# Optimization experiments

Measured on AMD Instinct MI355X. Metric: run time of the kernel, lower is better.

The kernel has to match this reference:

```python
import jax, jax.numpy as jnp
import numpy as np

NG, NT, E = 2500, 20000, 640000
SRC_DIM, DST_DIM, HID, OUT, NCLS = 128, 500, 128, 128, 16


def setup_inputs() -> dict:
    key = jax.random.key(0)
    ks = jax.random.split(key, 11)
    d = {
        "gene_feats": jax.random.normal(ks[0], (NG, SRC_DIM), jnp.float32),
        "train_feats": jax.random.normal(ks[1], (NT, DST_DIM), jnp.float32),
        "edge_src": jax.random.randint(ks[2], (E,), 0, NG),
        "edge_dst": jax.random.randint(ks[3], (E,), 0, NT),
        # conv1: SAGEConv((src_dim, dst_dim) -> hidden)
        "W1_neigh": jax.random.normal(ks[4], (SRC_DIM, HID), jnp.float32) / np.sqrt(SRC_DIM),
        "W1_self": jax.random.normal(ks[5], (DST_DIM, HID), jnp.float32) / np.sqrt(DST_DIM),
        "b1": jnp.zeros((HID,), jnp.float32),
        # conv2: SAGEConv(hidden -> out); src input is the raw gene features
        "W2_neigh": jax.random.normal(ks[6], (HID, OUT), jnp.float32) / np.sqrt(HID),
        "W2_self": jax.random.normal(ks[7], (HID, OUT), jnp.float32) / np.sqrt(HID),
        "b2": jnp.zeros((OUT,), jnp.float32),
        # classifier MLP
        "Wc1": jax.random.normal(ks[8], (OUT, OUT), jnp.float32) / np.sqrt(OUT),
        "bc1": jnp.zeros((OUT,), jnp.float32),
        "Wc2": jax.random.normal(ks[9], (OUT, NCLS), jnp.float32) / np.sqrt(OUT),
        "bc2": jnp.zeros((NCLS,), jnp.float32),
    }
    return d


def _segment_mean(msgs, dst, num_segments):
    # mean over in-edges; isolated dst nodes get 0 (DGL convention)
    sums = jax.ops.segment_sum(msgs, dst, num_segments=num_segments)
    cnt = jax.ops.segment_sum(jnp.ones((msgs.shape[0],), msgs.dtype), dst,
                              num_segments=num_segments)
    return sums / jnp.maximum(cnt, 1.0)[:, None]


def reference(gene_feats, train_feats, edge_src, edge_dst,
              W1_neigh, W1_self, b1, W2_neigh, W2_self, b2,
              Wc1, bc1, Wc2, bc2):
    # mean-aggregate gene (src) features onto train (dst) nodes
    agg = _segment_mean(gene_feats[edge_src], edge_dst, NT)  # [NT, SRC_DIM]
    # conv1: fc_self(h_dst) + fc_neigh(mean_neigh) + bias, then ReLU
    h1 = jax.nn.relu(train_feats @ W1_self + agg @ W1_neigh + b1)  # [NT, HID]
    # conv2 reuses raw gene features as src -> same mean aggregation
    h2 = jax.nn.relu(h1 @ W2_self + agg @ W2_neigh + b2)  # [NT, OUT]
    # classifier: Linear -> ReLU -> Linear
    return jax.nn.relu(h2 @ Wc1 + bc1) @ Wc2 + bc2  # [NT, NCLS]
```

## Files before the change

### kernel.cpp

```cpp
#include <hip/hip_runtime.h>


#define NG 2500
#define NT 20000
#define NE 640000
#define NCLS 16
#define CAP 96

typedef unsigned short u16;
typedef unsigned int u32;

typedef float f32x4 __attribute__((ext_vector_type(4)));
typedef __bf16 bf16x8 __attribute__((ext_vector_type(8)));

__device__ __forceinline__ float b2f(u16 u) { return __uint_as_float(((u32)u) << 16); }
__device__ __forceinline__ float blo(u32 p) { return __uint_as_float(p << 16); }
__device__ __forceinline__ float bhi(u32 p) { return __uint_as_float(p & 0xffff0000u); }
__device__ __forceinline__ u16 f2b(float f) {
    u32 u = __float_as_uint(f);
    return (u16)((u + 0x7fffu + ((u >> 16) & 1u)) >> 16);
}

#define B1N 81920
#define B2N 32768
#define B3N 16384
#define B4N 2048
#define NEB 625
#define GNB 625
#define PKB 520

__global__ __launch_bounds__(256) void k_prep(
    const int* __restrict__ esrc, const int* __restrict__ edst,
    int* __restrict__ cnt, u16* __restrict__ csr,
    const float* __restrict__ gene, u32* __restrict__ GH32,
    const float* __restrict__ W1n, const float* __restrict__ W1s,
    const float* __restrict__ W2n, const float* __restrict__ W2s,
    const float* __restrict__ Wc1, const float* __restrict__ Wc2,
    u16* __restrict__ B1h, u16* __restrict__ B1l,
    u16* __restrict__ B2h, u16* __restrict__ B2l,
    u16* __restrict__ B3h, u16* __restrict__ B3l,
    u16* __restrict__ B4h, u16* __restrict__ B4l) {
    int blk = blockIdx.x, t = threadIdx.x;
    if (blk < NEB) {
        int e0 = (blk * 256 + t) * 4;
        const int4 s4 = *(const int4*)(esrc + e0);
        const int4 d4 = *(const int4*)(edst + e0);
        int ss[4] = {s4.x, s4.y, s4.z, s4.w};
        int dd[4] = {d4.x, d4.y, d4.z, d4.w};
#pragma unroll
        for (int i = 0; i < 4; ++i) {
            unsigned d = (unsigned)dd[i];
            if (d < NT) {
                int slot = atomicAdd(&cnt[d], 1);
                if (slot < CAP) csr[(size_t)d * CAP + slot] = (u16)ss[i];
            }
        }
        return;
    }
    if (blk < NEB + GNB) {
        int idx = (blk - NEB) * 256 + t;
        float2 v = ((const float2*)gene)[idx];
        GH32[idx] = (u32)f2b(v.x) | ((u32)f2b(v.y) << 16);
        return;
    }
    int idx = (blk - NEB - GNB) * 256 + t;
    float v = 0.f;
    u16 *ph = 0, *pl = 0;
    int off = 0;
    if (idx < B1N) {
        int j = idx & 7, l = (idx >> 3) & 63, rest = idx >> 9;
        int g = rest & 7, kk = rest >> 3;
        int k = kk * 32 + ((l >> 4) << 3) + j, n = (g << 4) + (l & 15);
        if (k < 500) v = W1s[k * 128 + n];
        else if (k >= 512) v = W1n[(k - 512) * 128 + n];
        ph = B1h; pl = B1l; off = idx;
    } else if (idx < B1N + B2N) {
        int e = idx - B1N;
        int j = e & 7, l = (e >> 3) & 63, rest = e >> 9;
        int g = rest & 7, kk = rest >> 3;
        int k = kk * 32 + ((l >> 4) << 3) + j, n = (g << 4) + (l & 15);
        v = (k < 128) ? W2s[k * 128 + n] : W2n[(k - 128) * 128 + n];
        ph = B2h; pl = B2l; off = e;
    } else if (idx < B1N + B2N + B3N) {
        int e = idx - (B1N + B2N);
        int j = e & 7, l = (e >> 3) & 63, rest = e >> 9;
        int g = rest & 7, kk = rest >> 3;
        int k = kk * 32 + ((l >> 4) << 3) + j, n = (g << 4) + (l & 15);
        v = Wc1[k * 128 + n];
        ph = B3h; pl = B3l; off = e;
    } else if (idx < B1N + B2N + B3N + B4N) {
        int e = idx - (B1N + B2N + B3N);
        int j = e & 7, l = (e >> 3) & 63, kk = e >> 9;
        int k = kk * 32 + ((l >> 4) << 3) + j, n = l & 15;
        v = Wc2[k * 16 + n];
        ph = B4h; pl = B4l; off = e;
    }
    if (ph) {
        u16 hi = f2b(v);
        u16 lo = f2b(v - b2f(hi));
        ph[off] = hi;
        pl[off] = lo;
    }
}

__global__ __launch_bounds__(512, 3) void k_mega(
    const int* __restrict__ cnt, const u16* __restrict__ csr,
    const u16* __restrict__ GH, const float* __restrict__ train,
    const u16* __restrict__ B1h, const u16* __restrict__ B1l,
    const u16* __restrict__ B2h, const u16* __restrict__ B2l,
    const u16* __restrict__ B3h, const u16* __restrict__ B3l,
    const u16* __restrict__ B4h, const u16* __restrict__ B4l,
    const float* __restrict__ b1, const float* __restrict__ b2,
    const float* __restrict__ bc1, const float* __restrict__ bc2,
    float* __restrict__ out) {
    __shared__ __align__(16) u16 SMEM[26112];
    u16* SAGh = SMEM;
    u16* SAGl = SMEM + 4352;
    u16* S1h = SMEM + 8704;
    u16* S1l = SMEM + 13056;
    u16* S2h = SMEM + 17408;
    u16* S2l = SMEM + 21760;
    u16* TS = SMEM + 8704;

    int t = threadIdx.x;
    int row0 = blockIdx.x * 32;

    float4 st[8];
    {
        const float4* tb = (const float4*)(train + (size_t)row0 * 500);
#pragma unroll
        for (int i = 0; i < 7; ++i) st[i] = tb[t + i * 512];
        if (t < 416) st[7] = tb[t + 3584];
    }

    int gr = t >> 4, cg = t & 15;
    int d = row0 + gr;
    int ctrue = cnt[d];
    int c = ctrue > CAP ? CAP : ctrue;
    const u16* crow = csr + (size_t)d * CAP;
    int nfull = c >> 3;
    uint4 i40 = *(const uint4*)(crow);
    uint4 i41 = *(const uint4*)(crow + 8);
    uint4 i42 = *(const uint4*)(crow + 16);
    uint4 i43 = *(const uint4*)(crow + 24);
    float a[8];
#pragma unroll
    for (int p = 0; p < 8; ++p) a[p] = 0.f;

    {
        u32* T32 = (u32*)TS;
#pragma unroll
        for (int i = 0; i < 8; ++i) {
            int idx = t + i * 512;
            if (i == 7 && t >= 416) break;
            int r = idx / 125, c4 = idx - r * 125;
            int base = r * 260 + c4 * 2;
            T32[base] = (u32)f2b(st[i].x) | ((u32)f2b(st[i].y) << 16);
            T32[base + 1] = (u32)f2b(st[i].z) | ((u32)f2b(st[i].w) << 16);
        }
        if (t < 192) {
            int r = t / 6, c4 = t - r * 6;
            T32[r * 260 + 250 + c4] = 0;
        }
    }
    __syncthreads();

    int lane = t & 63, g = t >> 6;
    int m = lane & 15, q = lane >> 4, n16 = lane & 15;

    int hr0 = m * 136 + q * 8;
    int hr1 = (16 + m) * 136 + q * 8;
    int cr0 = q * 4, cr1 = 16 + q * 4;
    const f32x4 z4 = {0.f, 0.f, 0.f, 0.f};
    f32x4 acc0 = z4, acc1 = z4;
    const u16* tA0 = TS + m * 520 + q * 8;
    const u16* tA1 = TS + (16 + m) * 520 + q * 8;

#define ACC(p)                                      \
    do {                                            \
        a[0] += blo((p).x); a[1] += bhi((p).x);     \
        a[2] += blo((p).y); a[3] += bhi((p).y);     \
        a[4] += blo((p).z); a[5] += bhi((p).z);     \
        a[6] += blo((p).w); a[7] += bhi((p).w);     \
    } while (0)

    auto GHLoad = [&](int s) -> uint4 {
        return *(const uint4*)(GH + (size_t)s * 128 + cg * 8);
    };
    uint4 P0, P1, P2, P3, P4, P5, P6, P7;
    auto issue8 = [&](uint4 iq) {
        P0 = GHLoad((int)(iq.x & 0xffffu)); P1 = GHLoad((int)(iq.x >> 16));
        P2 = GHLoad((int)(iq.y & 0xffffu)); P3 = GHLoad((int)(iq.y >> 16));
        P4 = GHLoad((int)(iq.z & 0xffffu)); P5 = GHLoad((int)(iq.z >> 16));
        P6 = GHLoad((int)(iq.w & 0xffffu)); P7 = GHLoad((int)(iq.w >> 16));
    };
    auto acc8 = [&]() {
        ACC(P0); ACC(P1); ACC(P2); ACC(P3);
        ACC(P4); ACC(P5); ACC(P6); ACC(P7);
    };
    auto kk4 = [&](int base) {
#pragma unroll
        for (int kk = base; kk < base + 4; ++kk) {
            bf16x8 a0 = *(const bf16x8*)(tA0 + kk * 32);
            bf16x8 a1 = *(const bf16x8*)(tA1 + kk * 32);
            size_t bo = ((size_t)(kk * 8 + g) * 64 + lane) * 8;
            bf16x8 bh = *(const bf16x8*)(B1h + bo);
            bf16x8 bl = *(const bf16x8*)(B1l + bo);
            acc0 = __builtin_amdgcn_mfma_f32_16x16x32_bf16(a0, bh, acc0, 0, 0, 0);
            acc0 = __builtin_amdgcn_mfma_f32_16x16x32_bf16(a0, bl, acc0, 0, 0, 0);
            acc1 = __builtin_amdgcn_mfma_f32_16x16x32_bf16(a1, bh, acc1, 0, 0, 0);
            acc1 = __builtin_amdgcn_mfma_f32_16x16x32_bf16(a1, bl, acc1, 0, 0, 0);
        }
    };

    if (nfull > 0) issue8(i40);
    kk4(0);
    if (nfull > 0) acc8();
    if (nfull > 1) issue8(i41);
    kk4(4);
    if (nfull > 1) acc8();
    if (nfull > 2) issue8(i42);
    kk4(8);
    if (nfull > 2) acc8();
    if (nfull > 3) issue8(i43);
    kk4(12);
    if (nfull > 3) acc8();
    for (int b = 4; b < nfull; ++b) {
        uint4 i4 = *(const uint4*)(crow + b * 8);
        issue8(i4);
        acc8();
    }
    {
        int j = nfull * 8;
        if (j < c) {
            uint4 i4 = *(const uint4*)(crow + j);
            u32 w[4] = {i4.x, i4.y, i4.z, i4.w};
#pragma unroll
            for (int k = 0; k < 8; ++k) {
                int s = (int)((w[k >> 1] >> ((k & 1) * 16)) & 0xffffu);
                bool live = (j + k) < c;
                s = live ? s : 0;
                uint4 p = GHLoad(s);
                if (live) ACC(p);
            }
        }
    }
#undef ACC

    {
        float inv = (ctrue > 0) ? 1.f / (float)ctrue : 0.f;
        int base = (gr * 136 + cg * 8) >> 1;
        u32* SH = (u32*)SAGh;
        u32* SL = (u32*)SAGl;
#pragma unroll
        for (int p = 0; p < 4; ++p) {
            float x = a[2 * p] * inv, y = a[2 * p + 1] * inv;
            u16 hx = f2b(x), hy = f2b(y);
            SH[base + p] = (u32)hx | ((u32)hy << 16);
            SL[base + p] = (u32)f2b(x - b2f(hx)) | ((u32)f2b(y - b2f(hy)) << 16);
        }
    }
    __syncthreads();

#pragma unroll
    for (int kk = 16; kk < 20; ++kk) {
        int o = (kk - 16) * 32;
        bf16x8 ah0 = *(const bf16x8*)(SAGh + hr0 + o);
        bf16x8 al0 = *(const bf16x8*)(SAGl + hr0 + o);
        bf16x8 ah1 = *(const bf16x8*)(SAGh + hr1 + o);
        bf16x8 al1 = *(const bf16x8*)(SAGl + hr1 + o);
        size_t bo = ((size_t)(kk * 8 + g) * 64 + lane) * 8;
        bf16x8 bh = *(const bf16x8*)(B1h + bo);
        bf16x8 bl = *(const bf16x8*)(B1l + bo);
        acc0 = __builtin_amdgcn_mfma_f32_16x16x32_bf16(ah0, bh, acc0, 0, 0, 0);
        acc0 = __builtin_amdgcn_mfma_f32_16x16x32_bf16(ah0, bl, acc0, 0, 0, 0);
        acc0 = __builtin_amdgcn_mfma_f32_16x16x32_bf16(al0, bh, acc0, 0, 0, 0);
        acc1 = __builtin_amdgcn_mfma_f32_16x16x32_bf16(ah1, bh, acc1, 0, 0, 0);
        acc1 = __builtin_amdgcn_mfma_f32_16x16x32_bf16(ah1, bl, acc1, 0, 0, 0);
        acc1 = __builtin_amdgcn_mfma_f32_16x16x32_bf16(al1, bh, acc1, 0, 0, 0);
    }
    {
        int n = g * 16 + n16;
        float bias = b1[n];
#pragma unroll
        for (int rg = 0; rg < 4; ++rg) {
            float v0 = acc0[rg] + bias; v0 = v0 > 0.f ? v0 : 0.f;
            float v1 = acc1[rg] + bias; v1 = v1 > 0.f ? v1 : 0.f;
            u16 h0 = f2b(v0), h1v = f2b(v1);
            S1h[(cr0 + rg) * 136 + n] = h0; S1l[(cr0 + rg) * 136 + n] = f2b(v0 - b2f(h0));
            S1h[(cr1 + rg) * 136 + n] = h1v; S1l[(cr1 + rg) * 136 + n] = f2b(v1 - b2f(h1v));
        }
    }
    __syncthreads();

    acc0 = z4; acc1 = z4;
#pragma unroll
    for (int kk = 0; kk < 8; ++kk) {
        const u16* Ph = (kk < 4) ? S1h : SAGh;
        const u16* Pl = (kk < 4) ? S1l : SAGl;
        int o = (kk & 3) * 32;
        bf16x8 ah0 = *(const bf16x8*)(Ph + hr0 + o);
        bf16x8 al0 = *(const bf16x8*)(Pl + hr0 + o);
        bf16x8 ah1 = *(const bf16x8*)(Ph + hr1 + o);
        bf16x8 al1 = *(const bf16x8*)(Pl + hr1 + o);
        size_t bo = ((size_t)(kk * 8 + g) * 64 + lane) * 8;
        bf16x8 bh = *(const bf16x8*)(B2h + bo);
        bf16x8 bl = *(const bf16x8*)(B2l + bo);
        acc0 = __builtin_amdgcn_mfma_f32_16x16x32_bf16(ah0, bh, acc0, 0, 0, 0);
        acc0 = __builtin_amdgcn_mfma_f32_16x16x32_bf16(ah0, bl, acc0, 0, 0, 0);
        acc0 = __builtin_amdgcn_mfma_f32_16x16x32_bf16(al0, bh, acc0, 0, 0, 0);
        acc1 = __builtin_amdgcn_mfma_f32_16x16x32_bf16(ah1, bh, acc1, 0, 0, 0);
        acc1 = __builtin_amdgcn_mfma_f32_16x16x32_bf16(ah1, bl, acc1, 0, 0, 0);
        acc1 = __builtin_amdgcn_mfma_f32_16x16x32_bf16(al1, bh, acc1, 0, 0, 0);
    }
    {
        int n = g * 16 + n16;
        float bias = b2[n];
#pragma unroll
        for (int rg = 0; rg < 4; ++rg) {
            float v0 = acc0[rg] + bias; v0 = v0 > 0.f ? v0 : 0.f;
            float v1 = acc1[rg] + bias; v1 = v1 > 0.f ? v1 : 0.f;
            u16 h0 = f2b(v0), h1v = f2b(v1);
            S2h[(cr0 + rg) * 136 + n] = h0; S2l[(cr0 + rg) * 136 + n] = f2b(v0 - b2f(h0));
            S2h[(cr1 + rg) * 136 + n] = h1v; S2l[(cr1 + rg) * 136 + n] = f2b(v1 - b2f(h1v));
        }
    }
    __syncthreads();

    acc0 = z4; acc1 = z4;
#pragma unroll
    for (int kk = 0; kk < 4; ++kk) {
        int o = kk * 32;
        bf16x8 ah0 = *(const bf16x8*)(S2h + hr0 + o);
        bf16x8 al0 = *(const bf16x8*)(S2l + hr0 + o);
        bf16x8 ah1 = *(const bf16x8*)(S2h + hr1 + o);
        bf16x8 al1 = *(const bf16x8*)(S2l + hr1 + o);
        size_t bo = ((size_t)(kk * 8 + g) * 64 + lane) * 8;
        bf16x8 bh = *(const bf16x8*)(B3h + bo);
        bf16x8 bl = *(const bf16x8*)(B3l + bo);
        acc0 = __builtin_amdgcn_mfma_f32_16x16x32_bf16(ah0, bh, acc0, 0, 0, 0);
        acc0 = __builtin_amdgcn_mfma_f32_16x16x32_bf16(ah0, bl, acc0, 0, 0, 0);
        acc0 = __builtin_amdgcn_mfma_f32_16x16x32_bf16(al0, bh, acc0, 0, 0, 0);
        acc1 = __builtin_amdgcn_mfma_f32_16x16x32_bf16(ah1, bh, acc1, 0, 0, 0);
        acc1 = __builtin_amdgcn_mfma_f32_16x16x32_bf16(ah1, bl, acc1, 0, 0, 0);
        acc1 = __builtin_amdgcn_mfma_f32_16x16x32_bf16(al1, bh, acc1, 0, 0, 0);
    }
    {
        int n = g * 16 + n16;
        float bias = bc1[n];
#pragma unroll
        for (int rg = 0; rg < 4; ++rg) {
            float v0 = acc0[rg] + bias; v0 = v0 > 0.f ? v0 : 0.f;
            float v1 = acc1[rg] + bias; v1 = v1 > 0.f ? v1 : 0.f;
            u16 h0 = f2b(v0), h1v = f2b(v1);
            S1h[(cr0 + rg) * 136 + n] = h0; S1l[(cr0 + rg) * 136 + n] = f2b(v0 - b2f(h0));
            S1h[(cr1 + rg) * 136 + n] = h1v; S1l[(cr1 + rg) * 136 + n] = f2b(v1 - b2f(h1v));
        }
    }
    __syncthreads();

    if (g < 2) {
        int hr = (g == 0) ? hr0 : hr1;
        int cr = (g == 0) ? cr0 : cr1;
        f32x4 a4 = z4;
#pragma unroll
        for (int kk = 0; kk < 4; ++kk) {
            bf16x8 ah = *(const bf16x8*)(S1h + hr + kk * 32);
            bf16x8 al = *(const bf16x8*)(S1l + hr + kk * 32);
            size_t bo = ((size_t)kk * 64 + lane) * 8;
            bf16x8 bh = *(const bf16x8*)(B4h + bo);
            bf16x8 bl = *(const bf16x8*)(B4l + bo);
            a4 = __builtin_amdgcn_mfma_f32_16x16x32_bf16(ah, bh, a4, 0, 0, 0);
            a4 = __builtin_amdgcn_mfma_f32_16x16x32_bf16(ah, bl, a4, 0, 0, 0);
            a4 = __builtin_amdgcn_mfma_f32_16x16x32_bf16(al, bh, a4, 0, 0, 0);
        }
        float bias = bc2[n16];
#pragma unroll
        for (int rg = 0; rg < 4; ++rg)
            out[(size_t)(row0 + cr + rg) * NCLS + n16] = a4[rg] + bias;
    }
}

extern "C" void kernel_launch(void* const* d_in, const int* in_sizes, int n_in,
                              void* d_out, int out_size, void* d_ws, size_t ws_size,
                              hipStream_t stream) {
    const float* gene = (const float*)d_in[0];
    const float* train = (const float*)d_in[1];
    const int* esrc = (const int*)d_in[2];
    const int* edst = (const int*)d_in[3];

    char* ws = (char*)d_ws;
    int* cnt = (int*)(ws + 0);
    u16* csr = (u16*)(ws + 80000);
    u16* GH = (u16*)(ws + 3920000);
    u16* B1h = (u16*)(ws + 4560000);
    u16* B1l = (u16*)(ws + 4723840);
    u16* B2h = (u16*)(ws + 4887680);
    u16* B2l = (u16*)(ws + 4953216);
    u16* B3h = (u16*)(ws + 5018752);
    u16* B3l = (u16*)(ws + 5051520);
    u16* B4h = (u16*)(ws + 5084288);
    u16* B4l = (u16*)(ws + 5088384);

    hipMemsetAsync(cnt, 0, NT * sizeof(int), stream);
    k_prep<<<NEB + GNB + PKB, 256, 0, stream>>>(
        esrc, edst, cnt, csr, gene, (u32*)GH,
        (const float*)d_in[4], (const float*)d_in[5], (const float*)d_in[7],
        (const float*)d_in[8], (const float*)d_in[10], (const float*)d_in[12],
        B1h, B1l, B2h, B2l, B3h, B3l, B4h, B4l);
    k_mega<<<NT / 32, 512, 0, stream>>>(
        cnt, csr, GH, train, B1h, B1l, B2h, B2l, B3h, B3l, B4h, B4l,
        (const float*)d_in[6], (const float*)d_in[9], (const float*)d_in[11],
        (const float*)d_in[13], (float*)d_out);
}
```

Baseline: 172.5 us.

## Bucket edges per 32-row block and build per-row lists in shared memory

Result: slower. 313.0 us (+81.5%).

```diff
diff --git a/kernel.cpp b/kernel.cpp
--- a/kernel.cpp
+++ b/kernel.cpp
@@ -6,6 +6,7 @@
 #define NE 640000
 #define NCLS 16
 #define CAP 96
+#define BCAP 1536
 
 typedef unsigned short u16;
 typedef unsigned int u32;
@@ -31,7 +32,7 @@
 
 __global__ __launch_bounds__(256) void k_prep(
     const int* __restrict__ esrc, const int* __restrict__ edst,
-    int* __restrict__ cnt, u16* __restrict__ csr,
+    int* __restrict__ bcnt, u32* __restrict__ bkt,
     const float* __restrict__ gene, u32* __restrict__ GH32,
     const float* __restrict__ W1n, const float* __restrict__ W1s,
     const float* __restrict__ W2n, const float* __restrict__ W2s,
@@ -51,8 +52,10 @@
         for (int i = 0; i < 4; ++i) {
             unsigned d = (unsigned)dd[i];
             if (d < NT) {
-                int slot = atomicAdd(&cnt[d], 1);
-                if (slot < CAP) csr[(size_t)d * CAP + slot] = (u16)ss[i];
+                int b = (int)(d >> 5);
+                int pos = atomicAdd(&bcnt[b], 1);
+                if (pos < BCAP)
+                    bkt[(size_t)b * BCAP + pos] = ((d & 31u) << 16) | (u32)ss[i];
             }
         }
         return;
@@ -104,7 +107,7 @@
 }
 
 __global__ __launch_bounds__(512, 3) void k_mega(
-    const int* __restrict__ cnt, const u16* __restrict__ csr,
+    const int* __restrict__ bcnt, const u32* __restrict__ bkt,
     const u16* __restrict__ GH, const float* __restrict__ train,
     const u16* __restrict__ B1h, const u16* __restrict__ B1l,
     const u16* __restrict__ B2h, const u16* __restrict__ B2l,
@@ -114,6 +117,8 @@
     const float* __restrict__ bc1, const float* __restrict__ bc2,
     float* __restrict__ out) {
     __shared__ __align__(16) u16 SMEM[26112];
+    __shared__ __align__(16) u16 SRT[32 * CAP];
+    __shared__ int POS[32];
     u16* SAGh = SMEM;
     u16* SAGl = SMEM + 4352;
     u16* S1h = SMEM + 8704;
@@ -133,19 +138,17 @@
         if (t < 416) st[7] = tb[t + 3584];
     }
 
-    int gr = t >> 4, cg = t & 15;
-    int d = row0 + gr;
-    int ctrue = cnt[d];
-    int c = ctrue > CAP ? CAP : ctrue;
-    const u16* crow = csr + (size_t)d * CAP;
-    int nfull = c >> 3;
-    uint4 i40 = *(const uint4*)(crow);
-    uint4 i41 = *(const uint4*)(crow + 8);
-    uint4 i42 = *(const uint4*)(crow + 16);
-    uint4 i43 = *(const uint4*)(crow + 24);
-    float a[8];
-#pragma unroll
-    for (int p = 0; p < 8; ++p) a[p] = 0.f;
+    if (t < 32) POS[t] = 0;
+    int bc = bcnt[blockIdx.x];
+    if (bc > BCAP) bc = BCAP;
+    __syncthreads();
+
+    for (int i = t; i < bc; i += 512) {
+        u32 e = bkt[(size_t)blockIdx.x * BCAP + i];
+        int r = (int)(e >> 16);
+        int p = atomicAdd(&POS[r], 1);
+        if (p < CAP) SRT[r * CAP + p] = (u16)(e & 0xffffu);
+    }
 
     {
         u32* T32 = (u32*)TS;
@@ -167,6 +170,19 @@
 
     int lane = t & 63, g = t >> 6;
     int m = lane & 15, q = lane >> 4, n16 = lane & 15;
+    int gr = t >> 4, cg = t & 15;
+
+    int ctrue = POS[gr];
+    int c = ctrue > CAP ? CAP : ctrue;
+    const u16* crow = SRT + gr * CAP;
+    int nfull = c >> 3;
+    uint4 i40 = *(const uint4*)(crow);
+    uint4 i41 = *(const uint4*)(crow + 8);
+    uint4 i42 = *(const uint4*)(crow + 16);
+    uint4 i43 = *(const uint4*)(crow + 24);
+    float a[8];
+#pragma unroll
+    for (int p = 0; p < 8; ++p) a[p] = 0.f;
 
     int hr0 = m * 136 + q * 8;
     int hr1 = (16 + m) * 136 + q * 8;
@@ -390,26 +406,26 @@
     const int* edst = (const int*)d_in[3];
 
     char* ws = (char*)d_ws;
-    int* cnt = (int*)(ws + 0);
-    u16* csr = (u16*)(ws + 80000);
-    u16* GH = (u16*)(ws + 3920000);
-    u16* B1h = (u16*)(ws + 4560000);
-    u16* B1l = (u16*)(ws + 4723840);
-    u16* B2h = (u16*)(ws + 4887680);
-    u16* B2l = (u16*)(ws + 4953216);
-    u16* B3h = (u16*)(ws + 5018752);
-    u16* B3l = (u16*)(ws + 5051520);
-    u16* B4h = (u16*)(ws + 5084288);
-    u16* B4l = (u16*)(ws + 5088384);
-
-    hipMemsetAsync(cnt, 0, NT * sizeof(int), stream);
+    int* bcnt = (int*)(ws + 0);
+    u32* bkt = (u32*)(ws + 4096);
+    u16* GH = (u16*)(ws + 3844096);
+    u16* B1h = (u16*)(ws + 4484096);
+    u16* B1l = (u16*)(ws + 4647936);
+    u16* B2h = (u16*)(ws + 4811776);
+    u16* B2l = (u16*)(ws + 4877312);
+    u16* B3h = (u16*)(ws + 4942848);
+    u16* B3l = (u16*)(ws + 4975616);
+    u16* B4h = (u16*)(ws + 5008384);
+    u16* B4l = (u16*)(ws + 5012480);
+
+    hipMemsetAsync(bcnt, 0, NEB * sizeof(int), stream);
     k_prep<<<NEB + GNB + PKB, 256, 0, stream>>>(
-        esrc, edst, cnt, csr, gene, (u32*)GH,
+        esrc, edst, bcnt, bkt, gene, (u32*)GH,
         (const float*)d_in[4], (const float*)d_in[5], (const float*)d_in[7],
         (const float*)d_in[8], (const float*)d_in[10], (const float*)d_in[12],
         B1h, B1l, B2h, B2l, B3h, B3l, B4h, B4l);
     k_mega<<<NT / 32, 512, 0, stream>>>(
-        cnt, csr, GH, train, B1h, B1l, B2h, B2l, B3h, B3l, B4h, B4l,
+        bcnt, bkt, GH, train, B1h, B1l, B2h, B2l, B3h, B3l, B4h, B4l,
         (const float*)d_in[6], (const float*)d_in[9], (const float*)d_in[11],
         (const float*)d_in[13], (float*)d_out);
 }
```
